# Performance work log

Measured on AMD Instinct MI355X. Metric: run time of the kernel, lower is better.

## Reference

```python
import jax, jax.numpy as jnp
import numpy as np

T_IN, T_OUT, B, D, H, L = 257, 256, 256, 131, 256, 2


def lstm_cell(x, h, c, Wih, Whh, bih, bhh):
    # torch LSTMCell gate order: i, f, g, o
    z = x @ Wih.T + h @ Whh.T + bih + bhh
    i, f, g, o = jnp.split(z, 4, axis=-1)
    c_new = jax.nn.sigmoid(f) * c + jax.nn.sigmoid(i) * jnp.tanh(g)
    h_new = jax.nn.sigmoid(o) * jnp.tanh(c_new)
    return h_new, c_new


def setup_inputs() -> dict:
    key = jax.random.key(0)
    ks = jax.random.split(key, 22)
    s = 0.05  # weight scale, keeps gates in the linear-ish region
    d = {}
    d["X"] = jax.random.normal(ks[0], (T_IN, B, D), jnp.float32)
    d["Y"] = jax.random.normal(ks[1], (T_OUT, B, D), jnp.float32)
    shapes = {
        "enc_Wih0": (4 * H, D), "enc_Whh0": (4 * H, H), "enc_bih0": (4 * H,), "enc_bhh0": (4 * H,),
        "enc_Wih1": (4 * H, H), "enc_Whh1": (4 * H, H), "enc_bih1": (4 * H,), "enc_bhh1": (4 * H,),
        "dec_Wih0": (4 * H, D), "dec_Whh0": (4 * H, H), "dec_bih0": (4 * H,), "dec_bhh0": (4 * H,),
        "dec_Wih1": (4 * H, H), "dec_Whh1": (4 * H, H), "dec_bih1": (4 * H,), "dec_bhh1": (4 * H,),
        "lin_W": (D, H), "lin_b": (D,),
    }
    for i, (name, shp) in enumerate(shapes.items()):
        d[name] = jax.random.normal(ks[2 + i], shp, jnp.float32) * s
    return d


def _make_step(params, emit):
    def step(carry, x):
        hs, cs = carry
        inp = x
        new_h, new_c = [], []
        for l, (Wih, Whh, bih, bhh) in enumerate(params):
            h, c = lstm_cell(inp, hs[l], cs[l], Wih, Whh, bih, bhh)
            new_h.append(h)
            new_c.append(c)
            inp = h
        out = emit(inp) if emit is not None else None
        return (tuple(new_h), tuple(new_c)), out
    return step


def reference(X, Y, enc_Wih0, enc_Whh0, enc_bih0, enc_bhh0,
              enc_Wih1, enc_Whh1, enc_bih1, enc_bhh1,
              dec_Wih0, dec_Whh0, dec_bih0, dec_bhh0,
              dec_Wih1, dec_Whh1, dec_bih1, dec_bhh1,
              lin_W, lin_b):
    enc = [(enc_Wih0, enc_Whh0, enc_bih0, enc_bhh0),
           (enc_Wih1, enc_Whh1, enc_bih1, enc_bhh1)]
    dec = [(dec_Wih0, dec_Whh0, dec_bih0, dec_bhh0),
           (dec_Wih1, dec_Whh1, dec_bih1, dec_bhh1)]
    b = X.shape[1]
    zeros = tuple(jnp.zeros((b, H), X.dtype) for _ in range(L))
    # encoder over X[:-1]
    (hn, cn), _ = jax.lax.scan(_make_step(enc, None), (zeros, zeros), X[:-1])
    # decoder (teacher forcing): inputs are [X[-1], Y[0], ..., Y[T_out-2]]
    dec_in = jnp.concatenate([X[-1:], Y[:-1]], axis=0)
    emit = lambda h: jax.nn.log_softmax(h @ lin_W.T + lin_b, axis=-1)
    _, Ypred = jax.lax.scan(_make_step(dec, emit), (hn, cn), dec_in)
    return Ypred  # (T_out, B, out_dim) log-probabilities
```

## Files before the change

### kernel.cpp

```cpp
#include <hip/hip_runtime.h>
#include <hip/hip_bf16.h>
#include <math.h>

typedef __attribute__((ext_vector_type(8))) short short8;
typedef __attribute__((ext_vector_type(4))) float f32x4;
typedef unsigned long long u64;

#define STEPS 512
#define BB 256
#define HH 256
#define DD 131
#define XP 160
#define K0P 416
#define KS0 424
#define K1  512
#define KS1 520
#define HS0 264
#define HS1 520
#define RING 16
#define PO   8
#define NGRP 8
#define ROWS 32
#define SLOT_E (ROWS * HH)
#define RGELEM (RING * SLOT_E)
#define POISON64 0x7F807F807F807F80ull

#define OFF_W0E 0
#define OFF_W0D (OFF_W0E + 1024 * K0P)
#define OFF_W1E (OFF_W0D + 1024 * K0P)
#define OFF_W1D (OFF_W1E + 1024 * K1)
#define OFF_LW  (OFF_W1D + 1024 * K1)
#define OFF_XBF (OFF_LW + 160 * 256)
#define OFF_H0R (OFF_XBF + (size_t)STEPS * BB * XP)
#define OFF_H1R (OFF_H0R + (size_t)NGRP * RGELEM)
#define OFF_H1A (OFF_H1R + (size_t)NGRP * RGELEM)
#define OFF_BF16_END (OFF_H1A + (size_t)256 * BB * HH)

#define LDS_W_OFF  0
#define LDS_HS_OFF 66560
#define LDS_TOTAL  133120

__device__ __forceinline__ float rcp_(float x) { return __builtin_amdgcn_rcpf(x); }
__device__ __forceinline__ float fsigm(float x) { return rcp_(1.f + __expf(-x)); }
__device__ __forceinline__ float ftanh(float x) {
    float t = __expf(-2.f * fabsf(x));
    float r = (1.f - t) * rcp_(1.f + t);
    return copysignf(r, x);
}
__device__ __forceinline__ u64 aload(const u64* p) {
    return __hip_atomic_load(p, __ATOMIC_RELAXED, __HIP_MEMORY_SCOPE_AGENT);
}
__device__ __forceinline__ void astore(u64* p, u64 v) {
    __hip_atomic_store(p, v, __ATOMIC_RELAXED, __HIP_MEMORY_SCOPE_AGENT);
}
__device__ __forceinline__ void astore16(unsigned short* p, unsigned short v) {
    __hip_atomic_store(p, v, __ATOMIC_RELAXED, __HIP_MEMORY_SCOPE_AGENT);
}
__device__ __forceinline__ bool haspoison(u64 v) {
    return (((v      ) & 0xFFFFull) == 0x7F80ull) ||
           (((v >> 16) & 0xFFFFull) == 0x7F80ull) ||
           (((v >> 32) & 0xFFFFull) == 0x7F80ull) ||
           (((v >> 48)           ) == 0x7F80ull);
}

__global__ __launch_bounds__(256) void pack_w0(const float* __restrict__ Wih,
                                               const float* __restrict__ Whh,
                                               __hip_bfloat16* __restrict__ dst) {
    int idx = blockIdx.x * 256 + threadIdx.x;
    int p = idx / K0P, k = idx - p * K0P;
    int ct = p >> 6, local = p & 63, g = local >> 4, j = local & 15;
    int orow = g * 256 + ct * 16 + j;
    float v = 0.f;
    if (k < DD) v = Wih[orow * DD + k];
    else if (k >= XP) v = Whh[orow * HH + (k - XP)];
    dst[idx] = __float2bfloat16(v);
}

__global__ __launch_bounds__(256) void pack_w1(const float* __restrict__ Wih,
                                               const float* __restrict__ Whh,
                                               __hip_bfloat16* __restrict__ dst) {
    int idx = blockIdx.x * 256 + threadIdx.x;
    int p = idx >> 9, k = idx & 511;
    int ct = p >> 6, local = p & 63, g = local >> 4, j = local & 15;
    int orow = g * 256 + ct * 16 + j;
    float v = (k < HH) ? Wih[orow * HH + k] : Whh[orow * HH + (k - HH)];
    dst[idx] = __float2bfloat16(v);
}

__global__ __launch_bounds__(256) void pack_bias(const float* __restrict__ bih,
                                                 const float* __restrict__ bhh,
                                                 float* __restrict__ dst) {
    int idx = blockIdx.x * 256 + threadIdx.x;
    if (idx < 1024) dst[idx] = bih[idx] + bhh[idx];
}

__global__ __launch_bounds__(256) void pack_xbf(const float* __restrict__ X,
                                                const float* __restrict__ Y,
                                                __hip_bfloat16* __restrict__ dst) {
    int idx = blockIdx.x * 256 + threadIdx.x;
    int kp = idx % XP;
    int rb = idx / XP;
    int b = rb & 255, s = rb >> 8;
    const float* src;
    if (s <= 256) src = X + ((size_t)s * BB + b) * DD;
    else          src = Y + ((size_t)(s - 257) * BB + b) * DD;
    dst[idx] = __float2bfloat16(kp < DD ? src[kp] : 0.f);
}

__global__ __launch_bounds__(256) void pack_linw(const float* __restrict__ linW,
                                                 __hip_bfloat16* __restrict__ dst) {
    int idx = blockIdx.x * 256 + threadIdx.x;
    int j = idx >> 8, k = idx & 255;
    dst[idx] = __float2bfloat16(j < DD ? linW[j * HH + k] : 0.f);
}

__global__ __launch_bounds__(256) void pack_linb(const float* __restrict__ linb,
                                                 float* __restrict__ dst) {
    int idx = threadIdx.x;
    if (idx < 160) dst[idx] = (idx < DD) ? linb[idx] : -1.0e30f;
}

__global__ __launch_bounds__(256) void init_rings(u64* __restrict__ rings,
                                                  int* __restrict__ acks) {
    int idx = blockIdx.x * 256 + threadIdx.x;
    if (idx < 2 * NGRP * (RGELEM / 4)) {
        int slot = (idx >> 11) & (RING - 1);
        rings[idx] = (slot == RING - 1) ? 0ull : POISON64;
    }
    if (idx < 256) acks[idx] = 0;
}

__global__ __launch_bounds__(512, 1) void lstm_persistent(
    const __hip_bfloat16* __restrict__ wsb,
    const float* __restrict__ bsum,
    __hip_bfloat16* __restrict__ h0ring,
    __hip_bfloat16* __restrict__ h1ring,
    __hip_bfloat16* __restrict__ h1all,
    int* __restrict__ acks) {
    extern __shared__ __align__(16) char lds[];
    __hip_bfloat16* Wlds = (__hip_bfloat16*)(lds + LDS_W_OFF);
    __hip_bfloat16* hst  = (__hip_bfloat16*)(lds + LDS_HS_OFF);

    const int tid = threadIdx.x;
    const int wg = blockIdx.x;
    const int xg = wg >> 5;
    const int slot_id = wg & 31;
    const int layer = slot_id >> 4;
    const int ct = slot_id & 15;
    const int lane = tid & 63;
    const int mt = tid >> 6;
    const int lrow = lane & 15;
    const int lk8 = (lane >> 4) * 8;
    const int crow = (lane >> 4) * 4;

    const int K  = layer ? K1 : K0P;
    const int KS = layer ? KS1 : KS0;
    const int HS = layer ? HS1 : HS0;
    int* ackp = acks + xg * 32;

    auto load_w = [&](int ph2) {
        const __hip_bfloat16* src = wsb +
            (layer ? (ph2 ? OFF_W1D : OFF_W1E) : (ph2 ? OFF_W0D : OFF_W0E)) +
            (size_t)ct * 64 * K;
        const int KC = K >> 3;
        for (int e = tid; e < 64 * KC; e += 512) {
            int p = e / KC, kc = e - p * KC;
            *(short8*)&Wlds[p * KS + kc * 8] =
                *(const short8*)&src[(size_t)p * K + kc * 8];
        }
    };
    load_w(0);

    const int jcol = ct * 16 + lrow;
    float br[2][4];
    #pragma unroll
    for (int ph = 0; ph < 2; ++ph)
        #pragma unroll
        for (int g = 0; g < 4; ++g)
            br[ph][g] = bsum[ph * 2048 + layer * 1024 + g * 256 + jcol];
    f32x4 creg = {0.f, 0.f, 0.f, 0.f};

    const __hip_bfloat16* Xbf = wsb + OFF_XBF;
    __hip_bfloat16* h0g = h0ring + (size_t)xg * RGELEM;
    __hip_bfloat16* h1g = h1ring + (size_t)xg * RGELEM;
    __hip_bfloat16* ringw = layer ? h1g : h0g;
    const int arow = mt * 16 + lrow;
    __syncthreads();

    for (int s = 0; s < STEPS; ++s) {
        const int ph = s >> 8;
        const bool defer_x = (s == 256);
        f32x4 acc[4];
        short8 xv[5];

        if (tid < 128) {
            #pragma unroll
            for (int g = 0; g < 4; ++g) acc[g] = (f32x4){0.f, 0.f, 0.f, 0.f};
            if (layer == 0) {
                const short8* xp = (const short8*)
                    &Xbf[((size_t)s * BB + xg * ROWS + arow) * XP];
                #pragma unroll
                for (int kt = 0; kt < 5; ++kt) xv[kt] = xp[kt * 4 + (lk8 >> 3)];
                if (!defer_x) {
                    #pragma unroll
                    for (int kt = 0; kt < 5; ++kt)
                        #pragma unroll
                        for (int g = 0; g < 4; ++g) {
                            short8 w = *(const short8*)
                                &Wlds[(g * 16 + lrow) * KS0 + kt * 32 + lk8];
                            acc[g] = __builtin_amdgcn_mfma_f32_16x16x32_bf16(
                                xv[kt], w, acc[g], 0, 0, 0);
                        }
                }
                if (tid == 127) {
                    int tgt = 16 * (s - (PO - 1));
                    if (tgt > 0) {
                        int guard = 0;
                        while (__hip_atomic_load(ackp, __ATOMIC_RELAXED,
                                                 __HIP_MEMORY_SCOPE_AGENT) < tgt) {
                            __builtin_amdgcn_s_sleep(1);
                            if (++guard > 65536) break;
                        }
                    }
                }
            }
        } else {
            const int ptid = tid - 128;
            __hip_bfloat16* hs = hst + (s & 1) * 32 * HS;
            if (layer == 0) {
                const u64* src = (const u64*)(h0g +
                    (size_t)((s + RING - 1) & (RING - 1)) * SLOT_E);
                u64 v[6];
                unsigned pend = 0;
                #pragma unroll
                for (int i = 0; i < 6; ++i)
                    if (ptid + i * 384 < 2048) pend |= (1u << i);
                int guard = 0;
                while (pend) {
                    #pragma unroll
                    for (int i = 0; i < 6; ++i)
                        if (pend & (1u << i)) v[i] = aload(src + ptid + i * 384);
                    unsigned np = 0;
                    #pragma unroll
                    for (int i = 0; i < 6; ++i)
                        if ((pend & (1u << i)) && haspoison(v[i])) np |= (1u << i);
                    pend = np;
                    if (pend) {
                        __builtin_amdgcn_s_sleep(1);
                        if (++guard > 65536) break;
                    }
                }
                #pragma unroll
                for (int i = 0; i < 6; ++i) {
                    int p = ptid + i * 384;
                    if (p < 2048) {
                        int row = p >> 6, c = p & 63;
                        *(u64*)&hs[row * HS0 + c * 4] = v[i];
                    }
                }
            } else {
                const u64* s0 = (const u64*)(h0g +
                    (size_t)(s & (RING - 1)) * SLOT_E);
                const u64* s1 = (const u64*)(h1g +
                    (size_t)((s + RING - 1) & (RING - 1)) * SLOT_E);
                u64 v[11];
                unsigned pend = 0;
                #pragma unroll
                for (int i = 0; i < 11; ++i)
                    if (ptid + i * 384 < 4096) pend |= (1u << i);
                int guard = 0;
                while (pend) {
                    #pragma unroll
                    for (int i = 0; i < 11; ++i)
                        if (pend & (1u << i)) {
                            int p = ptid + i * 384;
                            v[i] = aload(p < 2048 ? s0 + p : s1 + (p - 2048));
                        }
                    unsigned np = 0;
                    #pragma unroll
                    for (int i = 0; i < 11; ++i)
                        if ((pend & (1u << i)) && haspoison(v[i])) np |= (1u << i);
                    pend = np;
                    if (pend) {
                        __builtin_amdgcn_s_sleep(1);
                        if (++guard > 65536) break;
                    }
                }
                #pragma unroll
                for (int i = 0; i < 11; ++i) {
                    int p = ptid + i * 384;
                    if (p < 4096) {
                        int pr = p & 2047;
                        int row = pr >> 6, c = pr & 63;
                        *(u64*)&hs[row * HS1 + (p < 2048 ? 0 : 256) + c * 4] = v[i];
                    }
                }
            }
        }
        __syncthreads();
        if (s == 256) { load_w(1); __syncthreads(); }

        if (tid < 128) {
            if (layer == 1 && tid == 0)
                __hip_atomic_fetch_add(ackp, 1, __ATOMIC_RELAXED,
                                       __HIP_MEMORY_SCOPE_AGENT);
            const __hip_bfloat16* hs = hst + (s & 1) * 32 * HS;
            if (layer == 0) {
                if (defer_x) {
                    #pragma unroll
                    for (int kt = 0; kt < 5; ++kt)
                        #pragma unroll
                        for (int g = 0; g < 4; ++g) {
                            short8 w = *(const short8*)
                                &Wlds[(g * 16 + lrow) * KS0 + kt * 32 + lk8];
                            acc[g] = __builtin_amdgcn_mfma_f32_16x16x32_bf16(
                                xv[kt], w, acc[g], 0, 0, 0);
                        }
                }
                #pragma unroll
                for (int kt = 0; kt < 8; ++kt) {
                    short8 a = *(const short8*)&hs[arow * HS0 + kt * 32 + lk8];
                    #pragma unroll
                    for (int g = 0; g < 4; ++g) {
                        short8 w = *(const short8*)
                            &Wlds[(g * 16 + lrow) * KS0 + (5 + kt) * 32 + lk8];
                        acc[g] = __builtin_amdgcn_mfma_f32_16x16x32_bf16(
                            a, w, acc[g], 0, 0, 0);
                    }
                }
            } else {
                #pragma unroll
                for (int kt = 0; kt < 16; ++kt) {
                    short8 a = *(const short8*)&hs[arow * HS1 + kt * 32 + lk8];
                    #pragma unroll
                    for (int g = 0; g < 4; ++g) {
                        short8 w = *(const short8*)
                            &Wlds[(g * 16 + lrow) * KS1 + kt * 32 + lk8];
                        acc[g] = __builtin_amdgcn_mfma_f32_16x16x32_bf16(
                            a, w, acc[g], 0, 0, 0);
                    }
                }
            }

            unsigned short* rp = (unsigned short*)
                (ringw + (size_t)(s & (RING - 1)) * SLOT_E);
            #pragma unroll
            for (int r = 0; r < 4; ++r) {
                float zi = acc[0][r] + br[ph][0];
                float zf = acc[1][r] + br[ph][1];
                float zg = acc[2][r] + br[ph][2];
                float zo = acc[3][r] + br[ph][3];
                float ig = fsigm(zi), fg = fsigm(zf), og = fsigm(zo);
                float cn = fg * creg[r] + ig * ftanh(zg);
                creg[r] = cn;
                union { __hip_bfloat16 b; unsigned short u; } cvt;
                cvt.b = __float2bfloat16(og * ftanh(cn));
                int row = mt * 16 + crow + r;
                astore16(&rp[row * HH + jcol], cvt.u);
                if (layer == 1 && s >= 256)
                    h1all[((size_t)(s - 256) * BB + xg * ROWS + row) * HH + jcol]
                        = cvt.b;
            }
            {
                int prow = tid >> 2, q = tid & 3;
                astore((u64*)(ringw +
                       (size_t)((s + PO) & (RING - 1)) * SLOT_E)
                       + prow * 64 + ct * 4 + q, POISON64);
            }
        }
    }
}

__global__ __launch_bounds__(256) void emit_mfma(
    const __hip_bfloat16* __restrict__ h1all,
    const __hip_bfloat16* __restrict__ lW,
    const float* __restrict__ lb,
    float* __restrict__ out) {
    __shared__ float lbs[160];
    const int tid = threadIdx.x;
    const int wv = tid >> 6, lane = tid & 63;
    const int lrow = lane & 15, lk8 = (lane >> 4) * 8, crow = (lane >> 4) * 4;
    const int row0 = blockIdx.x * 64;
    if (tid < 160) lbs[tid] = lb[tid];
    __syncthreads();

    f32x4 acc[10];
    #pragma unroll
    for (int f = 0; f < 10; ++f) acc[f] = (f32x4){0.f, 0.f, 0.f, 0.f};
    const int arow = row0 + wv * 16 + lrow;
    #pragma unroll
    for (int kt = 0; kt < 8; ++kt) {
        short8 a = *reinterpret_cast<const short8*>(
            &h1all[(size_t)arow * HH + kt * 32 + lk8]);
        #pragma unroll
        for (int f = 0; f < 10; ++f) {
            short8 w = *reinterpret_cast<const short8*>(
                &lW[(size_t)(f * 16 + lrow) * HH + kt * 32 + lk8]);
            acc[f] = __builtin_amdgcn_mfma_f32_16x16x32_bf16(a, w, acc[f], 0, 0, 0);
        }
    }
    #pragma unroll
    for (int r = 0; r < 4; ++r) {
        float m = -3.0e38f;
        #pragma unroll
        for (int f = 0; f < 10; ++f) m = fmaxf(m, acc[f][r] + lbs[f * 16 + lrow]);
        #pragma unroll
        for (int d = 1; d < 16; d <<= 1) m = fmaxf(m, __shfl_xor(m, d, 64));
        float ss = 0.f;
        #pragma unroll
        for (int f = 0; f < 10; ++f) ss += __expf(acc[f][r] + lbs[f * 16 + lrow] - m);
        #pragma unroll
        for (int d = 1; d < 16; d <<= 1) ss += __shfl_xor(ss, d, 64);
        float lse = m + logf(ss);
        int grow = row0 + wv * 16 + crow + r;
        #pragma unroll
        for (int f = 0; f < 9; ++f) {
            int j = f * 16 + lrow;
            if (j < DD)
                out[(size_t)grow * DD + j] = acc[f][r] + lbs[j] - lse;
        }
    }
}

extern "C" void kernel_launch(void* const* d_in, const int* in_sizes, int n_in,
                              void* d_out, int out_size, void* d_ws, size_t ws_size,
                              hipStream_t stream) {
    const float* X     = (const float*)d_in[0];
    const float* Y     = (const float*)d_in[1];
    const float* eWih0 = (const float*)d_in[2];
    const float* eWhh0 = (const float*)d_in[3];
    const float* ebih0 = (const float*)d_in[4];
    const float* ebhh0 = (const float*)d_in[5];
    const float* eWih1 = (const float*)d_in[6];
    const float* eWhh1 = (const float*)d_in[7];
    const float* ebih1 = (const float*)d_in[8];
    const float* ebhh1 = (const float*)d_in[9];
    const float* dWih0 = (const float*)d_in[10];
    const float* dWhh0 = (const float*)d_in[11];
    const float* dbih0 = (const float*)d_in[12];
    const float* dbhh0 = (const float*)d_in[13];
    const float* dWih1 = (const float*)d_in[14];
    const float* dWhh1 = (const float*)d_in[15];
    const float* dbih1 = (const float*)d_in[16];
    const float* dbhh1 = (const float*)d_in[17];
    const float* linW  = (const float*)d_in[18];
    const float* linb  = (const float*)d_in[19];
    float* out = (float*)d_out;

    __hip_bfloat16* wsb = (__hip_bfloat16*)d_ws;
    float* freg  = (float*)(wsb + OFF_BF16_END);
    float* bsum  = freg;
    float* linbp = freg + 4096;
    int*   acks  = (int*)(freg + 4096 + 192);

    pack_w0<<<dim3(1664), dim3(256), 0, stream>>>(eWih0, eWhh0, wsb + OFF_W0E);
    pack_w0<<<dim3(1664), dim3(256), 0, stream>>>(dWih0, dWhh0, wsb + OFF_W0D);
    pack_w1<<<dim3(2048), dim3(256), 0, stream>>>(eWih1, eWhh1, wsb + OFF_W1E);
    pack_w1<<<dim3(2048), dim3(256), 0, stream>>>(dWih1, dWhh1, wsb + OFF_W1D);
    pack_bias<<<dim3(4), dim3(256), 0, stream>>>(ebih0, ebhh0, bsum + 0);
    pack_bias<<<dim3(4), dim3(256), 0, stream>>>(ebih1, ebhh1, bsum + 1024);
    pack_bias<<<dim3(4), dim3(256), 0, stream>>>(dbih0, dbhh0, bsum + 2048);
    pack_bias<<<dim3(4), dim3(256), 0, stream>>>(dbih1, dbhh1, bsum + 3072);
    pack_xbf<<<dim3(81920), dim3(256), 0, stream>>>(X, Y, wsb + OFF_XBF);
    pack_linw<<<dim3(160), dim3(256), 0, stream>>>(linW, wsb + OFF_LW);
    pack_linb<<<dim3(1), dim3(256), 0, stream>>>(linb, linbp);
    init_rings<<<dim3(2048), dim3(256), 0, stream>>>((u64*)(wsb + OFF_H0R), acks);

    hipFuncSetAttribute((const void*)lstm_persistent,
                        hipFuncAttributeMaxDynamicSharedMemorySize, LDS_TOTAL);
    lstm_persistent<<<dim3(256), dim3(512), LDS_TOTAL, stream>>>(
        wsb, bsum, wsb + OFF_H0R, wsb + OFF_H1R, wsb + OFF_H1A, acks);

    emit_mfma<<<dim3(1024), dim3(256), 0, stream>>>(wsb + OFF_H1A, wsb + OFF_LW,
                                                    linbp, out);
}
```

Measured before the change: 2.666 ms.

## Pack h outputs into 64-bit atomic stores via shuffles; move ack wait to producer thread

```diff
diff --git a/kernel.cpp b/kernel.cpp
--- a/kernel.cpp
+++ b/kernel.cpp
@@ -53,15 +53,6 @@
 __device__ __forceinline__ void astore(u64* p, u64 v) {
     __hip_atomic_store(p, v, __ATOMIC_RELAXED, __HIP_MEMORY_SCOPE_AGENT);
 }
-__device__ __forceinline__ void astore16(unsigned short* p, unsigned short v) {
-    __hip_atomic_store(p, v, __ATOMIC_RELAXED, __HIP_MEMORY_SCOPE_AGENT);
-}
-__device__ __forceinline__ bool haspoison(u64 v) {
-    return (((v      ) & 0xFFFFull) == 0x7F80ull) ||
-           (((v >> 16) & 0xFFFFull) == 0x7F80ull) ||
-           (((v >> 32) & 0xFFFFull) == 0x7F80ull) ||
-           (((v >> 48)           ) == 0x7F80ull);
-}
 
 __global__ __launch_bounds__(256) void pack_w0(const float* __restrict__ Wih,
                                                const float* __restrict__ Whh,
@@ -151,7 +142,6 @@
     const int mt = tid >> 6;
     const int lrow = lane & 15;
     const int lk8 = (lane >> 4) * 8;
-    const int crow = (lane >> 4) * 4;
 
     const int K  = layer ? K1 : K0P;
     const int KS = layer ? KS1 : KS0;
@@ -212,17 +202,6 @@
                                 xv[kt], w, acc[g], 0, 0, 0);
                         }
                 }
-                if (tid == 127) {
-                    int tgt = 16 * (s - (PO - 1));
-                    if (tgt > 0) {
-                        int guard = 0;
-                        while (__hip_atomic_load(ackp, __ATOMIC_RELAXED,
-                                                 __HIP_MEMORY_SCOPE_AGENT) < tgt) {
-                            __builtin_amdgcn_s_sleep(1);
-                            if (++guard > 65536) break;
-                        }
-                    }
-                }
             }
         } else {
             const int ptid = tid - 128;
@@ -243,7 +222,8 @@
                     unsigned np = 0;
                     #pragma unroll
                     for (int i = 0; i < 6; ++i)
-                        if ((pend & (1u << i)) && haspoison(v[i])) np |= (1u << i);
+                        if ((pend & (1u << i)) &&
+                            ((v[i] & 0xFFFFull) == 0x7F80ull)) np |= (1u << i);
                     pend = np;
                     if (pend) {
                         __builtin_amdgcn_s_sleep(1);
@@ -256,6 +236,17 @@
                     if (p < 2048) {
                         int row = p >> 6, c = p & 63;
                         *(u64*)&hs[row * HS0 + c * 4] = v[i];
+                    }
+                }
+                if (ptid == 383) {
+                    int tgt = 16 * (s - (PO - 1));
+                    if (tgt > 0) {
+                        int guard2 = 0;
+                        while (__hip_atomic_load(ackp, __ATOMIC_RELAXED,
+                                                 __HIP_MEMORY_SCOPE_AGENT) < tgt) {
+                            __builtin_amdgcn_s_sleep(1);
+                            if (++guard2 > 65536) break;
+                        }
                     }
                 }
             } else {
@@ -279,7 +270,8 @@
                     unsigned np = 0;
                     #pragma unroll
                     for (int i = 0; i < 11; ++i)
-                        if ((pend & (1u << i)) && haspoison(v[i])) np |= (1u << i);
+                        if ((pend & (1u << i)) &&
+                            ((v[i] & 0xFFFFull) == 0x7F80ull)) np |= (1u << i);
                     pend = np;
                     if (pend) {
                         __builtin_amdgcn_s_sleep(1);
@@ -342,8 +334,7 @@
                 }
             }
 
-            unsigned short* rp = (unsigned short*)
-                (ringw + (size_t)(s & (RING - 1)) * SLOT_E);
+            unsigned short hu[4];
             #pragma unroll
             for (int r = 0; r < 4; ++r) {
                 float zi = acc[0][r] + br[ph][0];
@@ -355,17 +346,36 @@
                 creg[r] = cn;
                 union { __hip_bfloat16 b; unsigned short u; } cvt;
                 cvt.b = __float2bfloat16(og * ftanh(cn));
-                int row = mt * 16 + crow + r;
-                astore16(&rp[row * HH + jcol], cvt.u);
+                hu[r] = cvt.u;
+            }
+
+            {
+                const int m = lane & 15, g16 = lane >> 4;
+                const int srcbase = g16 * 16 + 4 * (m & 3);
+                const int myslot = m >> 2;
+                unsigned short pa = 0, pb = 0, pc = 0, pd = 0;
+                #pragma unroll
+                for (int rr = 0; rr < 4; ++rr) {
+                    int q0 = __shfl((int)hu[rr], srcbase + 0, 64);
+                    int q1 = __shfl((int)hu[rr], srcbase + 1, 64);
+                    int q2 = __shfl((int)hu[rr], srcbase + 2, 64);
+                    int q3 = __shfl((int)hu[rr], srcbase + 3, 64);
+                    if (myslot == rr) {
+                        pa = (unsigned short)q0; pb = (unsigned short)q1;
+                        pc = (unsigned short)q2; pd = (unsigned short)q3;
+                    }
+                }
+                u64 pkt = (u64)pa | ((u64)pb << 16) | ((u64)pc << 32)
+                        | ((u64)pd << 48);
+                const int prow = mt * 16 + g16 * 4 + myslot;
+                const int pq = m & 3;
+                astore((u64*)(ringw + (size_t)(s & (RING - 1)) * SLOT_E)
+                       + prow * 64 + ct * 4 + pq, pkt);
                 if (layer == 1 && s >= 256)
-                    h1all[((size_t)(s - 256) * BB + xg * ROWS + row) * HH + jcol]
-                        = cvt.b;
-            }
-            {
-                int prow = tid >> 2, q = tid & 3;
-                astore((u64*)(ringw +
-                       (size_t)((s + PO) & (RING - 1)) * SLOT_E)
-                       + prow * 64 + ct * 4 + q, POISON64);
+                    *(u64*)&h1all[((size_t)(s - 256) * BB + xg * ROWS + prow) * HH
+                                  + ct * 16 + pq * 4] = pkt;
+                astore((u64*)(ringw + (size_t)((s + PO) & (RING - 1)) * SLOT_E)
+                       + prow * 64 + ct * 4 + pq, POISON64);
             }
         }
     }
```

Result: faster. 2.470 ms (-7.4%).
